# Kernel tuning notes

Measured on AMD Instinct MI355X. Metric: run time of the kernel, lower is better.

Reference implementation:

```python
import jax, jax.numpy as jnp
import numpy as np

B, S = 2, 2048
D_MODEL, N_HEAD = 2048, 16
D_K = D_MODEL // N_HEAD        # 128
D_C, D_CQ = 512, 1024
D_ROPE = 64
D_NOPE = D_K - D_ROPE          # 64
EPS = 1.1920929e-07            # torch.finfo(float32).eps (nn.RMSNorm default)


def rms_norm(x, w):
    var = jnp.mean(x * x, axis=-1, keepdims=True)
    return x * jax.lax.rsqrt(var + EPS) * w


def setup_inputs() -> dict:
    key = jax.random.key(0)
    ks = jax.random.split(key, 16)
    g = lambda k, shape: (jax.random.normal(k, shape, dtype=jnp.float32) * 0.02)
    return {
        "x": jax.random.normal(ks[0], (B, S, D_MODEL), dtype=jnp.float32),
        "q_down_w": g(ks[1], (D_CQ, D_MODEL)),
        "q_down_b": g(ks[2], (D_CQ,)),
        "q_norm_w": jnp.ones((D_CQ,), jnp.float32),
        "q_up_w": g(ks[3], (N_HEAD * D_K, D_CQ)),
        "q_up_b": g(ks[4], (N_HEAD * D_K,)),
        "kv_down_w": g(ks[5], (D_C, D_MODEL)),
        "kv_down_b": g(ks[6], (D_C,)),
        "kv_norm_w": jnp.ones((D_C,), jnp.float32),
        "kv_up_w": g(ks[7], (N_HEAD * (D_NOPE + D_K), D_C)),
        "kv_up_b": g(ks[8], (N_HEAD * (D_NOPE + D_K),)),
        "k_rope_w": g(ks[9], (N_HEAD * D_ROPE, D_MODEL)),
        "k_rope_b": g(ks[10], (N_HEAD * D_ROPE,)),
        "out_w": g(ks[11], (D_MODEL, D_MODEL)),
        "out_b": g(ks[12], (D_MODEL,)),
    }


def reference(x, q_down_w, q_down_b, q_norm_w, q_up_w, q_up_b,
              kv_down_w, kv_down_b, kv_norm_w, kv_up_w, kv_up_b,
              k_rope_w, k_rope_b, out_w, out_b):
    b, s, _ = x.shape
    # Q low-rank path: down -> RMSNorm -> up
    c_q = rms_norm(x @ q_down_w.T + q_down_b, q_norm_w)              # [b,s,d_cq]
    q = (c_q @ q_up_w.T + q_up_b).reshape(b, s, N_HEAD, D_K)
    q = jnp.transpose(q, (0, 2, 1, 3))                               # [b,h,s,d_k]
    q_nope, q_rope = q[..., :D_NOPE], q[..., D_NOPE:]
    # KV low-rank path
    c_kv = rms_norm(x @ kv_down_w.T + kv_down_b, kv_norm_w)          # [b,s,d_c]
    kv = (c_kv @ kv_up_w.T + kv_up_b).reshape(b, s, N_HEAD, D_NOPE + D_K)
    kv = jnp.transpose(kv, (0, 2, 1, 3))                             # [b,h,s,d_nope+d_k]
    k_nope, v = kv[..., :D_NOPE], kv[..., D_NOPE:]
    # decoupled rope subspace (rope=None config: no rotation applied)
    k_rope = (x @ k_rope_w.T + k_rope_b).reshape(b, s, N_HEAD, D_ROPE)
    k_rope = jnp.transpose(k_rope, (0, 2, 1, 3))                     # [b,h,s,d_rope]
    q = jnp.concatenate([q_nope, q_rope], axis=-1)                   # [b,h,s,d_k]
    k = jnp.concatenate([k_nope, k_rope], axis=-1)                   # [b,h,s,d_k]
    # causal attention
    scores = jnp.einsum('bhnd,bhmd->bhnm', q, k) / np.sqrt(D_K).astype(np.float32)
    mask = jnp.tril(jnp.ones((s, s), dtype=bool))
    scores = jnp.where(mask, scores, -jnp.inf)
    probs = jax.nn.softmax(scores, axis=-1)
    attn = jnp.einsum('bhnm,bhmd->bhnd', probs, v)                   # [b,h,s,d_k]
    attn = jnp.transpose(attn, (0, 2, 1, 3)).reshape(b, s, D_MODEL)
    return attn @ out_w.T + out_b
```

## Files before the change

kernel.cpp:

```cpp
#include <hip/hip_runtime.h>
#include <hip/hip_bf16.h>

typedef __attribute__((ext_vector_type(8))) short bf16x8;
typedef __attribute__((ext_vector_type(4))) float f32x4;
typedef unsigned short u16;

#define RMS_EPS 1.1920929e-07f

constexpr int Bb = 2, Ss = 2048, DM = 2048, NH = 16;
constexpr int MROWS = Bb * Ss;

__device__ __forceinline__ u16 f2bf(float f) {
    __hip_bfloat16 h = __float2bfloat16(f);
    return *reinterpret_cast<u16*>(&h);
}

__device__ __forceinline__ float exp2_fast(float x) {
    float r; asm("v_exp_f32 %0, %1" : "=v"(r) : "v"(x)); return r;
}

__device__ __forceinline__ void gload16(const void* g, void* l) {
    __builtin_amdgcn_global_load_lds(
        (const __attribute__((address_space(1))) unsigned int*)g,
        (__attribute__((address_space(3))) unsigned int*)l, 16, 0, 0);
}

__global__ __launch_bounds__(256) void cvt_all(
    const float* __restrict__ s0, u16* __restrict__ d0,
    const float* __restrict__ s1, u16* __restrict__ d1,
    const float* __restrict__ s2, u16* __restrict__ d2,
    const float* __restrict__ s3, u16* __restrict__ d3,
    const float* __restrict__ s4, u16* __restrict__ d4,
    const float* __restrict__ s5, u16* __restrict__ d5,
    const float* __restrict__ s6, u16* __restrict__ d6)
{
    int i = blockIdx.x * 256 + threadIdx.x;
    const float* s; u16* d; int off;
    if (i < 2097152)      { s = s0; d = d0; off = 0; }
    else if (i < 2621440) { s = s1; d = d1; off = 2097152; }
    else if (i < 2883584) { s = s2; d = d2; off = 2621440; }
    else if (i < 3407872) { s = s3; d = d3; off = 2883584; }
    else if (i < 3932160) { s = s4; d = d4; off = 3407872; }
    else if (i < 4325376) { s = s5; d = d5; off = 3932160; }
    else                  { s = s6; d = d6; off = 4325376; }
    int j = i - off;
    float4 v = reinterpret_cast<const float4*>(s)[j];
    ushort4 o;
    o.x = f2bf(v.x); o.y = f2bf(v.y); o.z = f2bf(v.z); o.w = f2bf(v.w);
    reinterpret_cast<ushort4*>(d)[j] = o;
}

__global__ void build_bcat(const float* __restrict__ qb, const float* __restrict__ kvb,
                           const float* __restrict__ krb, float* __restrict__ bcat) {
    int i = blockIdx.x * 256 + threadIdx.x;
    if (i < 1024) bcat[i] = qb[i];
    else if (i < 1536) bcat[i] = kvb[i - 1024];
    else if (i < 2560) bcat[i] = krb[i - 1536];
}

template <typename OutT>
__global__ __launch_bounds__(256) void gemm_bt(
    const u16* __restrict__ A, const u16* __restrict__ Bt,
    const float* __restrict__ bias, OutT* __restrict__ C,
    int M, int N, int K)
{
    __shared__ alignas(16) u16 sA[128 * 32];
    __shared__ alignas(16) u16 sB[128 * 32];
    const int tid = threadIdx.x;
    const int lane = tid & 63;
    const int w = tid >> 6;
    const int wr = w >> 1, wc = w & 1;
    const int l16 = lane & 15, lq = lane >> 4;
    const int tileM = blockIdx.y * 128;
    const int tileN = blockIdx.x * 128;

    f32x4 acc[4][4];
#pragma unroll
    for (int m = 0; m < 4; m++)
#pragma unroll
        for (int n = 0; n < 4; n++)
#pragma unroll
            for (int r = 0; r < 4; r++) acc[m][n][r] = 0.f;

    const int srow = w * 16 + (lane >> 2);
    const int scol = (lane & 3) * 8;
    const u16* gA0 = A + (size_t)(tileM + srow) * K + scol;
    const u16* gA1 = A + (size_t)(tileM + srow + 64) * K + scol;
    const u16* gB0 = Bt + (size_t)(tileN + srow) * K + scol;
    const u16* gB1 = Bt + (size_t)(tileN + srow + 64) * K + scol;
    u16* lA0 = sA + w * 512;
    u16* lA1 = sA + 2048 + w * 512;
    u16* lB0 = sB + w * 512;
    u16* lB1 = sB + 2048 + w * 512;

    int aoff[4], boff[4];
#pragma unroll
    for (int m = 0; m < 4; m++) aoff[m] = (wr * 64 + m * 16 + l16) * 32 + lq * 8;
#pragma unroll
    for (int n = 0; n < 4; n++) boff[n] = (wc * 64 + n * 16 + l16) * 32 + lq * 8;

    const int nk = K >> 5;
    for (int kk = 0; kk < nk; ++kk) {
        __syncthreads();
        gload16(gA0, lA0);
        gload16(gA1, lA1);
        gload16(gB0, lB0);
        gload16(gB1, lB1);
        gA0 += 32; gA1 += 32; gB0 += 32; gB1 += 32;
        __syncthreads();
        bf16x8 af[4], bfr[4];
#pragma unroll
        for (int m = 0; m < 4; m++) af[m] = *(const bf16x8*)&sA[aoff[m]];
#pragma unroll
        for (int n = 0; n < 4; n++) bfr[n] = *(const bf16x8*)&sB[boff[n]];
        __builtin_amdgcn_s_setprio(1);
#pragma unroll
        for (int m = 0; m < 4; m++)
#pragma unroll
            for (int n = 0; n < 4; n++)
                acc[m][n] = __builtin_amdgcn_mfma_f32_16x16x32_bf16(af[m], bfr[n], acc[m][n], 0, 0, 0);
        __builtin_amdgcn_s_setprio(0);
    }

#pragma unroll
    for (int n = 0; n < 4; n++) {
        int col = tileN + wc * 64 + n * 16 + l16;
        float bv = bias ? bias[col] : 0.f;
#pragma unroll
        for (int m = 0; m < 4; m++) {
            int rowb = tileM + wr * 64 + m * 16 + (lq << 2);
#pragma unroll
            for (int r = 0; r < 4; r++) {
                float v = acc[m][n][r] + bv;
                if constexpr (sizeof(OutT) == 2)
                    C[(size_t)(rowb + r) * N + col] = (OutT)f2bf(v);
                else
                    C[(size_t)(rowb + r) * N + col] = (OutT)v;
            }
        }
    }
}

__global__ __launch_bounds__(256) void gemm_down(
    const u16* __restrict__ A, const u16* __restrict__ Bt,
    const float* __restrict__ bcat, float* __restrict__ dcat,
    u16* __restrict__ krbuf)
{
    constexpr int K = 2048;
    __shared__ alignas(16) u16 sA[128 * 32];
    __shared__ alignas(16) u16 sB[128 * 32];
    const int tid = threadIdx.x;
    const int lane = tid & 63;
    const int w = tid >> 6;
    const int wr = w >> 1, wc = w & 1;
    const int l16 = lane & 15, lq = lane >> 4;
    const int tileM = blockIdx.y * 128;
    const int tileN = blockIdx.x * 128;

    f32x4 acc[4][4];
#pragma unroll
    for (int m = 0; m < 4; m++)
#pragma unroll
        for (int n = 0; n < 4; n++)
#pragma unroll
            for (int r = 0; r < 4; r++) acc[m][n][r] = 0.f;

    const int srow = w * 16 + (lane >> 2);
    const int scol = (lane & 3) * 8;
    const u16* gA0 = A + (size_t)(tileM + srow) * K + scol;
    const u16* gA1 = A + (size_t)(tileM + srow + 64) * K + scol;
    const u16* gB0 = Bt + (size_t)(tileN + srow) * K + scol;
    const u16* gB1 = Bt + (size_t)(tileN + srow + 64) * K + scol;
    u16* lA0 = sA + w * 512;
    u16* lA1 = sA + 2048 + w * 512;
    u16* lB0 = sB + w * 512;
    u16* lB1 = sB + 2048 + w * 512;

    int aoff[4], boff[4];
#pragma unroll
    for (int m = 0; m < 4; m++) aoff[m] = (wr * 64 + m * 16 + l16) * 32 + lq * 8;
#pragma unroll
    for (int n = 0; n < 4; n++) boff[n] = (wc * 64 + n * 16 + l16) * 32 + lq * 8;

    const int nk = K >> 5;
    for (int kk = 0; kk < nk; ++kk) {
        __syncthreads();
        gload16(gA0, lA0);
        gload16(gA1, lA1);
        gload16(gB0, lB0);
        gload16(gB1, lB1);
        gA0 += 32; gA1 += 32; gB0 += 32; gB1 += 32;
        __syncthreads();
        bf16x8 af[4], bfr[4];
#pragma unroll
        for (int m = 0; m < 4; m++) af[m] = *(const bf16x8*)&sA[aoff[m]];
#pragma unroll
        for (int n = 0; n < 4; n++) bfr[n] = *(const bf16x8*)&sB[boff[n]];
        __builtin_amdgcn_s_setprio(1);
#pragma unroll
        for (int m = 0; m < 4; m++)
#pragma unroll
            for (int n = 0; n < 4; n++)
                acc[m][n] = __builtin_amdgcn_mfma_f32_16x16x32_bf16(af[m], bfr[n], acc[m][n], 0, 0, 0);
        __builtin_amdgcn_s_setprio(0);
    }

    const bool isrope = (tileN >= 1536);
#pragma unroll
    for (int n = 0; n < 4; n++) {
        int col = tileN + wc * 64 + n * 16 + l16;
        float bv = bcat[col];
#pragma unroll
        for (int m = 0; m < 4; m++) {
            int rowb = tileM + wr * 64 + m * 16 + (lq << 2);
#pragma unroll
            for (int r = 0; r < 4; r++) {
                float v = acc[m][n][r] + bv;
                if (!isrope) dcat[(size_t)(rowb + r) * 1536 + col] = v;
                else         krbuf[(size_t)(rowb + r) * 1024 + (col - 1536)] = f2bf(v);
            }
        }
    }
}

template <int C>
__global__ __launch_bounds__(256) void rmsnorm_bf16(
    const float* __restrict__ in, int istride, const float* __restrict__ wgt, u16* __restrict__ out)
{
    const int row = blockIdx.x;
    const int tid = threadIdx.x;
    constexpr int PER = C / 256;
    const float* p = in + (size_t)row * istride;
    float v[PER];
    float ss = 0.f;
#pragma unroll
    for (int i = 0; i < PER; i++) { v[i] = p[tid + i * 256]; ss += v[i] * v[i]; }
#pragma unroll
    for (int o = 32; o; o >>= 1) ss += __shfl_xor(ss, o, 64);
    __shared__ float red[4];
    if ((tid & 63) == 0) red[tid >> 6] = ss;
    __syncthreads();
    float tot = red[0] + red[1] + red[2] + red[3];
    float inv = rsqrtf(tot / (float)C + RMS_EPS);
    u16* q = out + (size_t)row * C;
#pragma unroll
    for (int i = 0; i < PER; i++) {
        int c = tid + i * 256;
        q[c] = f2bf(v[i] * inv * wgt[c]);
    }
}

__global__ __launch_bounds__(256) void transpose_v(
    const u16* __restrict__ kvbuf, u16* __restrict__ vT)
{
    __shared__ alignas(16) u16 tile[64][72];
    const int tid = threadIdx.x;
    const int t0 = blockIdx.x * 64;
    const int h = blockIdx.y >> 1, dh = blockIdx.y & 1;
    const int trow = tid >> 2, c8 = (tid & 3) * 8;
    const u16* src = kvbuf + (size_t)(t0 + trow) * 3072 + h * 192 + 64 + dh * 64 + c8;
    *(bf16x8*)&tile[trow][c8]      = *(const bf16x8*)src;
    *(bf16x8*)&tile[trow][c8 + 32] = *(const bf16x8*)(src + 32);
    __syncthreads();
    const int drow = tid >> 2, tc8 = (tid & 3) * 8;
    bf16x8 a, b2;
#pragma unroll
    for (int j = 0; j < 8; j++) {
        a[j]  = (short)tile[tc8 + j][drow];
        b2[j] = (short)tile[tc8 + 32 + j][drow];
    }
    u16* dst = vT + (size_t)(h * 128 + dh * 64 + drow) * MROWS + t0 + tc8;
    *(bf16x8*)dst = a;
    *(bf16x8*)(dst + 32) = b2;
}

__global__ __launch_bounds__(256) void mla_attn(
    const u16* __restrict__ qbuf,
    const u16* __restrict__ kvbuf,
    const u16* __restrict__ krbuf,
    const u16* __restrict__ vT,
    u16* __restrict__ obuf)
{
    const int flat = blockIdx.x + 8 * blockIdx.y;
    const int xcd = flat & 7, ii = flat >> 3;
    const int bh = xcd * 4 + (ii >> 3);
    const int p  = ii & 7;
    const int b = bh >> 4, h = bh & 15;
    const int tid = threadIdx.x, lane = tid & 63, w = tid >> 6;
    const int l16 = lane & 15, lq = lane >> 4;

    __shared__ alignas(16) u16 sK[64 * 128];
    __shared__ alignas(16) u16 sVt[128 * 64];
    __shared__ alignas(16) u16 sP[8][16 * 64];

    const int rowbase = b * Ss;
    const int sr = tid >> 2, sc = (tid & 3) * 32;
    const int vd = tid >> 1, vh = (tid & 1) * 32;
    const float C1 = 0.12751742f;
    const float THRR = 90.5f;

#pragma unroll 1
    for (int pass = 0; pass < 2; ++pass) {
        const int qt = pass ? (15 - p) : p;
        const int q0 = qt * 128;
        const int nkt = 2 * qt + 2;

        bf16x8 qf[2][4];
#pragma unroll
        for (int g = 0; g < 2; ++g) {
            const u16* qp = qbuf + (size_t)(rowbase + q0 + w * 32 + g * 16 + l16) * 2048 + h * 128 + lq * 8;
#pragma unroll
            for (int c = 0; c < 4; c++) qf[g][c] = *(const bf16x8*)(qp + c * 32);
        }
        float mi[2], li[2];
        f32x4 o[2][8];
#pragma unroll
        for (int g = 0; g < 2; ++g) {
            mi[g] = -3e38f; li[g] = 0.f;
#pragma unroll
            for (int d = 0; d < 8; d++)
#pragma unroll
                for (int r = 0; r < 4; r++) o[g][d][r] = 0.f;
        }

        bf16x8 kr[4], vr[4];
        {
            const int krow = rowbase + sr;
            const u16* src = (sc < 64)
                ? kvbuf + (size_t)krow * 3072 + h * 192 + sc
                : krbuf + (size_t)krow * 1024 + h * 64 + (sc - 64);
#pragma unroll
            for (int j = 0; j < 4; j++) kr[j] = *(const bf16x8*)(src + j * 8);
            const u16* vsrc = vT + (size_t)(h * 128 + vd) * MROWS + rowbase + vh;
#pragma unroll
            for (int j = 0; j < 4; j++) vr[j] = *(const bf16x8*)(vsrc + j * 8);
        }

        for (int kt = 0; kt < nkt; ++kt) {
            __syncthreads();
#pragma unroll
            for (int j = 0; j < 4; j++) {
                int byteoff = sr * 256 + (sc + j * 8) * 2;
                *(bf16x8*)((char*)sK + (byteoff ^ ((sr & 7) << 4))) = kr[j];
            }
#pragma unroll
            for (int j = 0; j < 4; j++) {
                int byteoff = vd * 128 + (vh + j * 8) * 2;
                *(bf16x8*)((char*)sVt + (byteoff ^ ((vd & 7) << 4))) = vr[j];
            }
            __syncthreads();
            if (kt + 1 < nkt) {
                const int krow = rowbase + (kt + 1) * 64 + sr;
                const u16* src = (sc < 64)
                    ? kvbuf + (size_t)krow * 3072 + h * 192 + sc
                    : krbuf + (size_t)krow * 1024 + h * 64 + (sc - 64);
#pragma unroll
                for (int j = 0; j < 4; j++) kr[j] = *(const bf16x8*)(src + j * 8);
                const u16* vsrc = vT + (size_t)(h * 128 + vd) * MROWS + rowbase + (kt + 1) * 64 + vh;
#pragma unroll
                for (int j = 0; j < 4; j++) vr[j] = *(const bf16x8*)(vsrc + j * 8);
            }

            const bool alive = (kt * 64) <= (q0 + w * 32 + 15);
            if (alive) {
                f32x4 scf[2][4];
#pragma unroll
                for (int g = 0; g < 2; ++g)
#pragma unroll
                    for (int n = 0; n < 4; n++)
#pragma unroll
                        for (int r = 0; r < 4; r++) scf[g][n][r] = 0.f;
                __builtin_amdgcn_s_setprio(1);
#pragma unroll
                for (int n = 0; n < 4; n++) {
#pragma unroll
                    for (int c = 0; c < 4; c++) {
                        int row = n * 16 + l16;
                        int byteoff = row * 256 + (c * 32 + lq * 8) * 2;
                        bf16x8 kf = *(const bf16x8*)((char*)sK + (byteoff ^ ((row & 7) << 4)));
                        scf[0][n] = __builtin_amdgcn_mfma_f32_16x16x32_bf16(kf, qf[0][c], scf[0][n], 0, 0, 0);
                        scf[1][n] = __builtin_amdgcn_mfma_f32_16x16x32_bf16(kf, qf[1][c], scf[1][n], 0, 0, 0);
                    }
                }
                __builtin_amdgcn_s_setprio(0);

#pragma unroll
                for (int g = 0; g < 2; ++g) {
                    const int base = q0 + w * 32 + g * 16;
                    if (kt * 64 + 63 > base) {
                        const int qg = base + l16;
#pragma unroll
                        for (int n = 0; n < 4; n++)
#pragma unroll
                            for (int r = 0; r < 4; r++) {
                                int kg = kt * 64 + n * 16 + lq * 4 + r;
                                if (kg > qg) scf[g][n][r] = -3e38f;
                            }
                    }
                    float mx = mi[g];
#pragma unroll
                    for (int n = 0; n < 4; n++)
#pragma unroll
                        for (int r = 0; r < 4; r++) mx = fmaxf(mx, scf[g][n][r]);
                    mx = fmaxf(mx, __shfl_xor(mx, 16, 64));
                    mx = fmaxf(mx, __shfl_xor(mx, 32, 64));
                    if (!__all(mx - mi[g] <= THRR)) {
                        float f = exp2_fast((mi[g] - mx) * C1);
                        li[g] *= f;
#pragma unroll
                        for (int d = 0; d < 8; d++)
#pragma unroll
                            for (int r = 0; r < 4; r++) o[g][d][r] *= f;
                        mi[g] = mx;
                    }
                    float mc = mi[g] * C1;
                    float rs = 0.f;
#pragma unroll
                    for (int n = 0; n < 4; n++)
#pragma unroll
                        for (int r = 0; r < 4; r++) {
                            float pv = exp2_fast(__fmaf_rn(scf[g][n][r], C1, -mc));
                            scf[g][n][r] = pv;
                            rs += pv;
                        }
                    rs += __shfl_xor(rs, 16, 64);
                    rs += __shfl_xor(rs, 32, 64);
                    li[g] += rs;
                    char* pb = (char*)sP + ((w << 1) | g) * 2048;
#pragma unroll
                    for (int n = 0; n < 4; n++) {
                        ushort4 pk;
                        pk.x = f2bf(scf[g][n][0]); pk.y = f2bf(scf[g][n][1]);
                        pk.z = f2bf(scf[g][n][2]); pk.w = f2bf(scf[g][n][3]);
                        int byteoff = l16 * 128 + n * 32 + lq * 8;
                        *(ushort4*)(pb + (byteoff ^ ((l16 & 7) << 4))) = pk;
                    }
                }

                __builtin_amdgcn_s_setprio(1);
#pragma unroll
                for (int c = 0; c < 2; c++) {
                    bf16x8 pf[2];
#pragma unroll
                    for (int g = 0; g < 2; ++g) {
                        char* pb = (char*)sP + ((w << 1) | g) * 2048;
                        int pbyte = l16 * 128 + (c * 32 + lq * 8) * 2;
                        pf[g] = *(const bf16x8*)(pb + (pbyte ^ ((l16 & 7) << 4)));
                    }
#pragma unroll
                    for (int d = 0; d < 8; d++) {
                        int vrow = d * 16 + l16;
                        int vbyte = vrow * 128 + (c * 32 + lq * 8) * 2;
                        bf16x8 vf = *(const bf16x8*)((char*)sVt + (vbyte ^ ((vrow & 7) << 4)));
                        o[0][d] = __builtin_amdgcn_mfma_f32_16x16x32_bf16(vf, pf[0], o[0][d], 0, 0, 0);
                        o[1][d] = __builtin_amdgcn_mfma_f32_16x16x32_bf16(vf, pf[1], o[1][d], 0, 0, 0);
                    }
                }
                __builtin_amdgcn_s_setprio(0);
            }
        }
#pragma unroll
        for (int g = 0; g < 2; ++g) {
            float invl = 1.f / li[g];
            u16* op = obuf + (size_t)(rowbase + q0 + w * 32 + g * 16 + l16) * 2048 + h * 128;
#pragma unroll
            for (int d = 0; d < 8; d++) {
                ushort4 ok;
                ok.x = f2bf(o[g][d][0] * invl); ok.y = f2bf(o[g][d][1] * invl);
                ok.z = f2bf(o[g][d][2] * invl); ok.w = f2bf(o[g][d][3] * invl);
                *(ushort4*)(op + d * 16 + lq * 4) = ok;
            }
        }
    }
}

extern "C" void kernel_launch(void* const* d_in, const int* in_sizes, int n_in,
                              void* d_out, int out_size, void* d_ws, size_t ws_size,
                              hipStream_t stream) {
    const float* x        = (const float*)d_in[0];
    const float* q_down_w = (const float*)d_in[1];
    const float* q_down_b = (const float*)d_in[2];
    const float* q_norm_w = (const float*)d_in[3];
    const float* q_up_w   = (const float*)d_in[4];
    const float* q_up_b   = (const float*)d_in[5];
    const float* kv_down_w= (const float*)d_in[6];
    const float* kv_down_b= (const float*)d_in[7];
    const float* kv_norm_w= (const float*)d_in[8];
    const float* kv_up_w  = (const float*)d_in[9];
    const float* kv_up_b  = (const float*)d_in[10];
    const float* k_rope_w = (const float*)d_in[11];
    const float* k_rope_b = (const float*)d_in[12];
    const float* out_w    = (const float*)d_in[13];
    const float* out_b    = (const float*)d_in[14];

    char* ws = (char*)d_ws;
    u16* xbf    = (u16*)(ws + 0);
    u16* wcat   = (u16*)(ws + 16777216);
    u16* quw    = (u16*)(ws + 27262976);
    u16* kvuw   = (u16*)(ws + 31457280);
    u16* outw   = (u16*)(ws + 34603008);
    float* bcat = (float*)(ws + 42991616);
    float* dcat = (float*)(ws + 43008000);
    u16* cq     = (u16*)(ws + 68173824);
    u16* ckv    = (u16*)(ws + 76562432);
    u16* qbuf   = (u16*)(ws + 80756736);
    u16* kvbuf  = (u16*)(ws + 97533952);
    u16* krbuf  = (u16*)(ws + 122699776);
    u16* vT     = (u16*)(ws + 0);
    u16* attnbuf= (u16*)(ws + 43008000);

    cvt_all<<<20992, 256, 0, stream>>>(
        x, xbf,
        q_down_w,  wcat,
        kv_down_w, wcat + 1024 * 2048,
        k_rope_w,  wcat + 1536 * 2048,
        q_up_w,    quw,
        kv_up_w,   kvuw,
        out_w,     outw);
    build_bcat<<<10, 256, 0, stream>>>(q_down_b, kv_down_b, k_rope_b, bcat);

    gemm_down<<<dim3(20, 32), 256, 0, stream>>>(xbf, wcat, bcat, dcat, krbuf);
    rmsnorm_bf16<1024><<<MROWS, 256, 0, stream>>>(dcat, 1536, q_norm_w, cq);
    rmsnorm_bf16<512><<<MROWS, 256, 0, stream>>>(dcat + 1024, 1536, kv_norm_w, ckv);
    gemm_bt<u16><<<dim3(16, 32), 256, 0, stream>>>(cq, quw, q_up_b, qbuf, MROWS, 2048, 1024);
    gemm_bt<u16><<<dim3(24, 32), 256, 0, stream>>>(ckv, kvuw, kv_up_b, kvbuf, MROWS, 3072, 512);
    transpose_v<<<dim3(64, 32), 256, 0, stream>>>(kvbuf, vT);
    mla_attn<<<dim3(8, 32), 256, 0, stream>>>(qbuf, kvbuf, krbuf, vT, attnbuf);
    gemm_bt<float><<<dim3(16, 32), 256, 0, stream>>>(attnbuf, outw, out_b, (float*)d_out, MROWS, 2048, 2048);
}
```

Baseline: 285.4 us.

## Split attention key range across two blocks per CU slot with split-K merge

The attention grid doubles from 256 to 512 blocks. Each original block's second (long, late) query tile is split along the key dimension: one half runs unmasked in the first block after its short tile, the other half runs masked in a new block. Partial outputs and (max, sum) statistics go to fp32 workspace and are combined by a new attn_merge kernel. This aims to fill more CUs and balance causal work, at the cost of extra fp32 partial traffic, an extra launch, and workspace aliasing that must not collide with live buffers.

```diff
diff --git a/kernel.cpp b/kernel.cpp
--- a/kernel.cpp
+++ b/kernel.cpp
@@ -279,13 +279,20 @@
     const u16* __restrict__ kvbuf,
     const u16* __restrict__ krbuf,
     const u16* __restrict__ vT,
-    u16* __restrict__ obuf)
+    u16* __restrict__ obuf,
+    float* __restrict__ part0,
+    float* __restrict__ p1a,
+    float* __restrict__ p1b,
+    float* __restrict__ ml)
 {
-    const int flat = blockIdx.x + 8 * blockIdx.y;
-    const int xcd = flat & 7, ii = flat >> 3;
+    const int flat = blockIdx.x + 16 * blockIdx.y;
+    const int cu_slot = flat & 255;
+    const int half = flat >> 8;
+    const int xcd = cu_slot & 7, ii = cu_slot >> 3;
     const int bh = xcd * 4 + (ii >> 3);
     const int p  = ii & 7;
     const int b = bh >> 4, h = bh & 15;
+    const int pi = bh * 8 + p;
     const int tid = threadIdx.x, lane = tid & 63, w = tid >> 6;
     const int l16 = lane & 15, lq = lane >> 4;
 
@@ -299,11 +306,16 @@
     const float C1 = 0.12751742f;
     const float THRR = 90.5f;
 
+    const int nseg = half ? 1 : 2;
 #pragma unroll 1
-    for (int pass = 0; pass < 2; ++pass) {
-        const int qt = pass ? (15 - p) : p;
+    for (int s = 0; s < nseg; ++s) {
+        int qt, k0, k1, mode;
+        bool domask;
+        if (half == 0) {
+            if (s == 0) { qt = p;      k0 = 0;          k1 = 2 * p + 2;  domask = true;  mode = 0; }
+            else        { qt = 15 - p; k0 = 0;          k1 = 15 - 2 * p; domask = false; mode = 1; }
+        } else          { qt = 15 - p; k0 = 15 - 2 * p; k1 = 32 - 2 * p; domask = true;  mode = 2; }
         const int q0 = qt * 128;
-        const int nkt = 2 * qt + 2;
 
         bf16x8 qf[2][4];
 #pragma unroll
@@ -325,18 +337,19 @@
 
         bf16x8 kr[4], vr[4];
         {
-            const int krow = rowbase + sr;
+            const int krow = rowbase + k0 * 64 + sr;
             const u16* src = (sc < 64)
                 ? kvbuf + (size_t)krow * 3072 + h * 192 + sc
                 : krbuf + (size_t)krow * 1024 + h * 64 + (sc - 64);
 #pragma unroll
             for (int j = 0; j < 4; j++) kr[j] = *(const bf16x8*)(src + j * 8);
-            const u16* vsrc = vT + (size_t)(h * 128 + vd) * MROWS + rowbase + vh;
+            const u16* vsrc = vT + (size_t)(h * 128 + vd) * MROWS + rowbase + k0 * 64 + vh;
 #pragma unroll
             for (int j = 0; j < 4; j++) vr[j] = *(const bf16x8*)(vsrc + j * 8);
         }
 
-        for (int kt = 0; kt < nkt; ++kt) {
+#pragma unroll 1
+        for (int kt = k0; kt < k1; ++kt) {
             __syncthreads();
 #pragma unroll
             for (int j = 0; j < 4; j++) {
@@ -349,7 +362,7 @@
                 *(bf16x8*)((char*)sVt + (byteoff ^ ((vd & 7) << 4))) = vr[j];
             }
             __syncthreads();
-            if (kt + 1 < nkt) {
+            if (kt + 1 < k1) {
                 const int krow = rowbase + (kt + 1) * 64 + sr;
                 const u16* src = (sc < 64)
                     ? kvbuf + (size_t)krow * 3072 + h * 192 + sc
@@ -361,7 +374,7 @@
                 for (int j = 0; j < 4; j++) vr[j] = *(const bf16x8*)(vsrc + j * 8);
             }
 
-            const bool alive = (kt * 64) <= (q0 + w * 32 + 15);
+            const bool alive = !domask || (kt * 64) <= (q0 + w * 32 + 15);
             if (alive) {
                 f32x4 scf[2][4];
 #pragma unroll
@@ -387,7 +400,7 @@
 #pragma unroll
                 for (int g = 0; g < 2; ++g) {
                     const int base = q0 + w * 32 + g * 16;
-                    if (kt * 64 + 63 > base) {
+                    if (domask && (kt * 64 + 63 > base)) {
                         const int qg = base + l16;
 #pragma unroll
                         for (int n = 0; n < 4; n++)
@@ -459,18 +472,72 @@
                 __builtin_amdgcn_s_setprio(0);
             }
         }
-#pragma unroll
-        for (int g = 0; g < 2; ++g) {
-            float invl = 1.f / li[g];
-            u16* op = obuf + (size_t)(rowbase + q0 + w * 32 + g * 16 + l16) * 2048 + h * 128;
-#pragma unroll
-            for (int d = 0; d < 8; d++) {
-                ushort4 ok;
-                ok.x = f2bf(o[g][d][0] * invl); ok.y = f2bf(o[g][d][1] * invl);
-                ok.z = f2bf(o[g][d][2] * invl); ok.w = f2bf(o[g][d][3] * invl);
-                *(ushort4*)(op + d * 16 + lq * 4) = ok;
+
+        if (mode == 0) {
+#pragma unroll
+            for (int g = 0; g < 2; ++g) {
+                float invl = 1.f / li[g];
+                u16* op = obuf + (size_t)(rowbase + q0 + w * 32 + g * 16 + l16) * 2048 + h * 128;
+#pragma unroll
+                for (int d = 0; d < 8; d++) {
+                    ushort4 ok;
+                    ok.x = f2bf(o[g][d][0] * invl); ok.y = f2bf(o[g][d][1] * invl);
+                    ok.z = f2bf(o[g][d][2] * invl); ok.w = f2bf(o[g][d][3] * invl);
+                    *(ushort4*)(op + d * 16 + lq * 4) = ok;
+                }
+            }
+        } else {
+            float* PB = (mode == 1)
+                ? part0 + (size_t)pi * 16384
+                : (pi < 192 ? p1a + (size_t)pi * 16384 : p1b + (size_t)(pi - 192) * 16384);
+            const int hslot = (mode == 2) ? 1 : 0;
+#pragma unroll
+            for (int g = 0; g < 2; ++g) {
+                const int rloc = w * 32 + g * 16 + l16;
+#pragma unroll
+                for (int d = 0; d < 8; d++)
+                    *(f32x4*)(PB + rloc * 128 + d * 16 + lq * 4) = o[g][d];
+                if (lq == 0) {
+                    float2 v; v.x = mi[g]; v.y = li[g];
+                    *(float2*)(ml + ((size_t)(pi * 2 + hslot) * 128 + rloc) * 2) = v;
+                }
             }
         }
+    }
+}
+
+__global__ __launch_bounds__(256) void attn_merge(
+    const float* __restrict__ part0, const float* __restrict__ p1a,
+    const float* __restrict__ p1b, const float* __restrict__ ml,
+    u16* __restrict__ obuf)
+{
+    const int pi = blockIdx.y;
+    const int quarter = blockIdx.x;
+    const int t = threadIdx.x;
+    const int r = quarter * 32 + (t >> 3);
+    const int d0 = (t & 7) * 16;
+    const int bh = pi >> 3, p = pi & 7, qt = 15 - p;
+    const int b = bh >> 4, h = bh & 15;
+    const float C1 = 0.12751742f;
+    float2 ml0 = *(const float2*)(ml + ((size_t)(pi * 2 + 0) * 128 + r) * 2);
+    float2 ml1 = *(const float2*)(ml + ((size_t)(pi * 2 + 1) * 128 + r) * 2);
+    float m = fmaxf(ml0.x, ml1.x);
+    float a0 = exp2_fast((ml0.x - m) * C1);
+    float a1 = exp2_fast((ml1.x - m) * C1);
+    float inv = 1.f / (ml0.y * a0 + ml1.y * a1);
+    const float* P0 = part0 + (size_t)pi * 16384 + r * 128 + d0;
+    const float* P1 = (pi < 192 ? p1a + (size_t)pi * 16384 : p1b + (size_t)(pi - 192) * 16384) + r * 128 + d0;
+    u16* dst = obuf + (size_t)(b * Ss + qt * 128 + r) * 2048 + h * 128 + d0;
+#pragma unroll
+    for (int j = 0; j < 4; j++) {
+        float4 o0 = *(const float4*)(P0 + j * 4);
+        float4 o1 = *(const float4*)(P1 + j * 4);
+        ushort4 ov;
+        ov.x = f2bf((o0.x * a0 + o1.x * a1) * inv);
+        ov.y = f2bf((o0.y * a0 + o1.y * a1) * inv);
+        ov.z = f2bf((o0.z * a0 + o1.z * a1) * inv);
+        ov.w = f2bf((o0.w * a0 + o1.w * a1) * inv);
+        *(ushort4*)(dst + j * 4) = ov;
     }
 }
 
@@ -508,6 +575,10 @@
     u16* krbuf  = (u16*)(ws + 122699776);
     u16* vT     = (u16*)(ws + 0);
     u16* attnbuf= (u16*)(ws + 43008000);
+    float* part0 = (float*)(ws + 16777216);
+    float* mlbuf = (float*)(ws + 33554432);
+    float* p1a   = (float*)(ws + 68173824);
+    float* p1b   = (float*)(ws + 59785216);
 
     cvt_all<<<20992, 256, 0, stream>>>(
         x, xbf,
@@ -525,6 +596,8 @@
     gemm_bt<u16><<<dim3(16, 32), 256, 0, stream>>>(cq, quw, q_up_b, qbuf, MROWS, 2048, 1024);
     gemm_bt<u16><<<dim3(24, 32), 256, 0, stream>>>(ckv, kvuw, kv_up_b, kvbuf, MROWS, 3072, 512);
     transpose_v<<<dim3(64, 32), 256, 0, stream>>>(kvbuf, vT);
-    mla_attn<<<dim3(8, 32), 256, 0, stream>>>(qbuf, kvbuf, krbuf, vT, attnbuf);
+    mla_attn<<<dim3(16, 32), 256, 0, stream>>>(qbuf, kvbuf, krbuf, vT, attnbuf,
+                                               part0, p1a, p1b, mlbuf);
+    attn_merge<<<dim3(4, 256), 256, 0, stream>>>(part0, p1a, p1b, mlbuf, attnbuf);
     gemm_bt<float><<<dim3(16, 32), 256, 0, stream>>>(attnbuf, outw, out_b, (float*)d_out, MROWS, 2048, 2048);
 }
```

Result: slower. 301.7 us (+5.7%).
